# Performance work log

Measured on AMD Instinct MI355X. Metric: run time of the kernel, lower is better.

Reference implementation:

```python
import jax, jax.numpy as jnp
import numpy as np

N, E, F_IN, DIM, HEADS, L, G, NC = 10000, 160000, 512, 256, 4, 3, 16, 10
HID = HEADS * DIM  # 1024


def gat_layer(x, src, dst, W, a_src, a_dst, b):
    # x: [N, in], W: [in, H*D], a_src/a_dst: [H, D], b: [H*D]
    h = (x @ W).reshape(N, HEADS, DIM)                       # [N,H,D]
    e_src = jnp.einsum('nhd,hd->nh', h, a_src)               # [N,H]
    e_dst = jnp.einsum('nhd,hd->nh', h, a_dst)               # [N,H]
    e = jax.nn.leaky_relu(e_src[src] + e_dst[dst], 0.2)      # [E,H]
    # segment softmax over edges grouped by destination node
    emax = jax.ops.segment_max(e, dst, num_segments=N)       # [N,H]
    ee = jnp.exp(e - emax[dst])
    denom = jax.ops.segment_sum(ee, dst, num_segments=N)     # [N,H]
    alpha = ee / denom[dst]                                  # [E,H]
    msg = h[src] * alpha[:, :, None]                         # [E,H,D]
    out = jax.ops.segment_sum(msg, dst, num_segments=N)      # [N,H,D]
    return out.reshape(N, HID) + b


def setup_inputs() -> dict:
    key = jax.random.key(0)
    ks = jax.random.split(key, 12)
    x = jax.random.normal(ks[0], (N, F_IN), dtype=jnp.float32)
    edge_index = jax.random.randint(ks[1], (2, E), 0, N, dtype=jnp.int32)
    batch = jnp.sort(jax.random.randint(ks[2], (N,), 0, G, dtype=jnp.int32))
    s0 = 1.0 / np.sqrt(F_IN)
    s1 = 1.0 / np.sqrt(HID)
    sd = 1.0 / np.sqrt(DIM)
    W0 = jax.random.normal(ks[3], (F_IN, HID), dtype=jnp.float32) * s0
    W1 = jax.random.normal(ks[4], (HID, HID), dtype=jnp.float32) * s1
    W2 = jax.random.normal(ks[5], (HID, HID), dtype=jnp.float32) * s1
    a_src = jax.random.normal(ks[6], (L, HEADS, DIM), dtype=jnp.float32) * sd
    a_dst = jax.random.normal(ks[7], (L, HEADS, DIM), dtype=jnp.float32) * sd
    bias = jnp.zeros((L, HID), dtype=jnp.float32)
    fc_w = jax.random.normal(ks[8], (HID, NC), dtype=jnp.float32) * s1
    fc_b = jnp.zeros((NC,), dtype=jnp.float32)
    return {"x": x, "edge_index": edge_index, "batch": batch, "W0": W0,
            "W1": W1, "W2": W2, "a_src": a_src, "a_dst": a_dst,
            "bias": bias, "fc_w": fc_w, "fc_b": fc_b}


def reference(x, edge_index, batch, W0, W1, W2, a_src, a_dst, bias, fc_w, fc_b):
    # add self-loops (PyG GATConv default)
    loop = jnp.arange(N, dtype=edge_index.dtype)
    src = jnp.concatenate([edge_index[0], loop])
    dst = jnp.concatenate([edge_index[1], loop])
    Ws = [W0, W1, W2]
    h = x
    for l in range(L):
        h = gat_layer(h, src, dst, Ws[l], a_src[l], a_dst[l], bias[l])
        h = jax.nn.relu(h)  # Dropout(0.5) is identity in eval mode
    # global mean pool over graphs
    sums = jax.ops.segment_sum(h, batch, num_segments=G)            # [G,HID]
    cnts = jax.ops.segment_sum(jnp.ones((N,), h.dtype), batch, num_segments=G)
    pooled = sums / jnp.maximum(cnts, 1.0)[:, None]
    logits = pooled @ fc_w + fc_b
    return jax.nn.log_softmax(logits, axis=-1)
```

## Files before the change

### kernel.cpp

```cpp
#include <hip/hip_runtime.h>
#include <math.h>

#define NNODES 10000
#define HID    1024
#define NHEADS 4
#define NGRAPH 16
#define NCLS   10

typedef __attribute__((ext_vector_type(8))) short bf16x8;
typedef __attribute__((ext_vector_type(8))) ushort u16x8;
typedef __attribute__((ext_vector_type(4))) float f32x4;
typedef __attribute__((ext_vector_type(2))) float f32x2;

__device__ __forceinline__ ushort bf16r(float f) {
    union { float f; unsigned u; } x; x.f = f;
    unsigned r = x.u + 0x7FFFu + ((x.u >> 16) & 1u);
    return (ushort)(r >> 16);
}
__device__ __forceinline__ float bf16f(ushort u) {
    union { unsigned u; float f; } x; x.u = ((unsigned)u) << 16;
    return x.f;
}
__device__ __forceinline__ float leaky(float e) { return e > 0.f ? e : 0.2f * e; }


__global__ void k_hist_conv(const int* __restrict__ dstArr, int* __restrict__ counts,
                            const int* __restrict__ batch, int* __restrict__ gstart,
                            int* __restrict__ gend, int E, int N,
                            const float* __restrict__ x, ushort* __restrict__ xb16, int n4) {
    int e = blockIdx.x * 256 + threadIdx.x;
    int total = E + N;
    if (e < total) {
        int d = (e < E) ? dstArr[e] : (e - E);
        atomicAdd(&counts[d], 1);
    }
    if (e < N) {
        int g = batch[e];
        if (e == 0 || batch[e - 1] != g) gstart[g] = e;
        if (e == N - 1 || batch[e + 1] != g) gend[g] = e + 1;
    }
    if (e < n4) {
        float4 v = ((const float4*)x)[e];
        ushort4 o;
        o.x = bf16r(v.x); o.y = bf16r(v.y); o.z = bf16r(v.z); o.w = bf16r(v.w);
        ((ushort4*)xb16)[e] = o;
    }
}

__global__ __launch_bounds__(1024) void k_scan(const int* __restrict__ counts,
                                               int* __restrict__ row_ptr, int N) {
    __shared__ int lds[1024];
    int t = threadIdx.x;
    const int C = (N + 1023) / 1024;
    int base = t * C;
    int s = 0;
    for (int i = 0; i < C; ++i)
        if (base + i < N) s += counts[base + i];
    lds[t] = s;
    __syncthreads();
    for (int off = 1; off < 1024; off <<= 1) {
        int add = (t >= off) ? lds[t - off] : 0;
        __syncthreads();
        lds[t] += add;
        __syncthreads();
    }
    int run = lds[t] - s;
    for (int i = 0; i < C; ++i) {
        if (base + i < N) {
            row_ptr[base + i] = run;
            run += counts[base + i];
        }
    }
    if (t == 1023) row_ptr[N] = lds[1023];
}

__global__ void k_scatter(const int* __restrict__ srcArr, const int* __restrict__ dstArr,
                          const int* __restrict__ row_ptr, int* __restrict__ fill,
                          int* __restrict__ col, int E) {
    int e = blockIdx.x * 256 + threadIdx.x;
    int total = E + NNODES;
    if (e < total) {
        int s, d;
        if (e < E) { s = srcArr[e]; d = dstArr[e]; }
        else       { s = d = e - E; }
        int pos = row_ptr[d] + atomicAdd(&fill[d], 1);
        col[pos] = s;
    }
}

__global__ __launch_bounds__(256) void k_wT3(const float* __restrict__ W0,
                                             const float* __restrict__ W1,
                                             const float* __restrict__ W2,
                                             ushort* __restrict__ w0t,
                                             ushort* __restrict__ w1t,
                                             ushort* __restrict__ w2t) {
    __shared__ ushort tile[32][33];
    int z = blockIdx.z;
    const float* W = (z == 0) ? W0 : (z == 1) ? W1 : W2;
    ushort* Wt     = (z == 0) ? w0t : (z == 1) ? w1t : w2t;
    int K          = (z == 0) ? 512 : HID;
    int bx = blockIdx.x;
    int by = blockIdx.y;
    if (by * 32 >= K) return;
    int tx = threadIdx.x & 31, ty = threadIdx.x >> 5;
#pragma unroll
    for (int i = 0; i < 32; i += 8) {
        int k  = by * 32 + ty + i;
        int nn = bx * 32 + tx;
        tile[ty + i][tx] = bf16r(W[(size_t)k * HID + nn]);
    }
    __syncthreads();
#pragma unroll
    for (int i = 0; i < 32; i += 8) {
        int nn = bx * 32 + ty + i;
        int k  = by * 32 + tx;
        Wt[(size_t)nn * K + k] = tile[tx][ty + i];
    }
}


#define BM 128
#define BN 128
#define BK 64

__global__ __launch_bounds__(256) void k_gemm_bf16(const ushort* __restrict__ A,
                                                   const ushort* __restrict__ Bt,
                                                   unsigned char* __restrict__ proj8,
                                                   int M, int K,
                                                   const float* __restrict__ asrcL,
                                                   const float* __restrict__ adstL,
                                                   float* __restrict__ esrcP,
                                                   float* __restrict__ edstP) {
    __shared__ ushort As[BM * BK];
    __shared__ ushort Bs[BN * BK];
    const int t    = threadIdx.x;
    const int lane = t & 63;
    const int w    = t >> 6;
    const int wr   = w >> 1, wc = w & 1;
    const int bm   = blockIdx.y * BM;
    const int bn   = blockIdx.x * BN;

    f32x4 acc[4][4] = {};

    const int r_  = t >> 3;
    const int cp_ = t & 7;

    const ushort* aSrc[4];
    const ushort* bSrc[4];
#pragma unroll
    for (int i = 0; i < 4; ++i) {
        int r  = i * 32 + r_;
        int c  = cp_ ^ (r & 7);
        int ga = bm + r; if (ga >= M) ga = M - 1;
        aSrc[i] = &A[(size_t)ga * K + c * 8];
        bSrc[i] = &Bt[(size_t)(bn + r) * K + c * 8];
    }

    for (int k0 = 0; k0 < K; k0 += BK) {
        __syncthreads();
#pragma unroll
        for (int i = 0; i < 4; ++i) {
            int fc = i * 256 + t;
            __builtin_amdgcn_global_load_lds(
                (const __attribute__((address_space(1))) unsigned*)(aSrc[i] + k0),
                (__attribute__((address_space(3))) unsigned*)&As[fc * 8], 16, 0, 0);
            __builtin_amdgcn_global_load_lds(
                (const __attribute__((address_space(1))) unsigned*)(bSrc[i] + k0),
                (__attribute__((address_space(3))) unsigned*)&Bs[fc * 8], 16, 0, 0);
        }
        __syncthreads();

#pragma unroll
        for (int s = 0; s < 2; ++s) {
            const int kc = s * 4 + (lane >> 4);
            bf16x8 a[4], b[4];
#pragma unroll
            for (int m = 0; m < 4; ++m) {
                int row = wr * 64 + m * 16 + (lane & 15);
                int ch  = kc ^ (row & 7);
                a[m] = *(const bf16x8*)&As[row * BK + ch * 8];
            }
#pragma unroll
            for (int n = 0; n < 4; ++n) {
                int cl = wc * 64 + n * 16 + (lane & 15);
                int ch = kc ^ (cl & 7);
                b[n] = *(const bf16x8*)&Bs[cl * BK + ch * 8];
            }
#pragma unroll
            for (int m = 0; m < 4; ++m)
#pragma unroll
                for (int n = 0; n < 4; ++n)
                    acc[m][n] = __builtin_amdgcn_mfma_f32_16x16x32_bf16(a[m], b[n], acc[m][n], 0, 0, 0);
        }
    }

    const int hcol0 = bn + wc * 64;
    const int slot  = hcol0 >> 6;
    float as_[4], ad_[4];
#pragma unroll
    for (int n = 0; n < 4; ++n) {
        int coln = hcol0 + n * 16 + (lane & 15);
        as_[n] = asrcL[coln];
        ad_[n] = adstL[coln];
    }
#pragma unroll
    for (int m = 0; m < 4; ++m) {
        int row0 = bm + wr * 64 + m * 16 + (lane >> 4) * 4;
#pragma unroll
        for (int j = 0; j < 4; ++j) {
            int row = row0 + j;
            float ps = 0.f, pd = 0.f;
#pragma unroll
            for (int n = 0; n < 4; ++n) {
                float v = acc[m][n][j];
                ps += v * as_[n];
                pd += v * ad_[n];
                if (row < M) {
                    int r8 = __builtin_amdgcn_cvt_pk_fp8_f32(v, v, 0, false);
                    proj8[(size_t)row * HID + hcol0 + n * 16 + (lane & 15)] =
                        (unsigned char)(r8 & 0xFF);
                }
            }
#pragma unroll
            for (int off = 1; off < 16; off <<= 1) {
                ps += __shfl_xor(ps, off);
                pd += __shfl_xor(pd, off);
            }
            if ((lane & 15) == 0 && row < M) {
                esrcP[row * 16 + slot] = ps;
                edstP[row * 16 + slot] = pd;
            }
        }
    }
}


__global__ __launch_bounds__(256) void k_agg(const unsigned char* __restrict__ proj8,
                                             const float* __restrict__ esrcP,
                                             const float* __restrict__ edstP,
                                             const int* __restrict__ row_ptr,
                                             const int* __restrict__ col,
                                             const float* __restrict__ bias,
                                             ushort* __restrict__ hb16) {
    __shared__ float aLds[4][64][NHEADS];

    const int nb   = threadIdx.x >> 6;
    const int nid  = blockIdx.x * 4 + nb;
    const int lane = threadIdx.x & 63;
    const int h    = lane >> 4;
    const int beg  = row_ptr[nid], end = row_ptr[nid + 1];
    const int deg  = end - beg;
    const bool fast = (deg <= 64);

    const float4* edP = (const float4*)&edstP[(size_t)nid * 16];
    float4 eda = edP[0], edb = edP[1], edc = edP[2], edd = edP[3];
    const float ed0 = eda.x + eda.y + eda.z + eda.w;
    const float ed1 = edb.x + edb.y + edb.z + edb.w;
    const float ed2 = edc.x + edc.y + edc.z + edc.w;
    const float ed3 = edd.x + edd.y + edd.z + edd.w;
    float invh;

    if (fast) {
        float e0[4];
        const bool has = lane < deg;
        float d0 = 0.f, d1 = 0.f, d2 = 0.f, d3 = 0.f;
        if (has) {
            const float4* eP = (const float4*)&esrcP[(size_t)col[beg + lane] * 16];
            float4 sa = eP[0], sb = eP[1], sc = eP[2], sd = eP[3];
            e0[0] = __expf(leaky(sa.x + sa.y + sa.z + sa.w + ed0)); d0 = e0[0];
            e0[1] = __expf(leaky(sb.x + sb.y + sb.z + sb.w + ed1)); d1 = e0[1];
            e0[2] = __expf(leaky(sc.x + sc.y + sc.z + sc.w + ed2)); d2 = e0[2];
            e0[3] = __expf(leaky(sd.x + sd.y + sd.z + sd.w + ed3)); d3 = e0[3];
        }
#pragma unroll
        for (int off = 32; off > 0; off >>= 1) {
            d0 += __shfl_xor(d0, off); d1 += __shfl_xor(d1, off);
            d2 += __shfl_xor(d2, off); d3 += __shfl_xor(d3, off);
        }
        if (has) {
            float4 a4 = make_float4(e0[0] / d0, e0[1] / d1, e0[2] / d2, e0[3] / d3);
            *(float4*)&aLds[nb][lane][0] = a4;
        }
    } else {
        float d0 = 0.f, d1 = 0.f, d2 = 0.f, d3 = 0.f;
        for (int j = beg + lane; j < end; j += 64) {
            const float4* eP = (const float4*)&esrcP[(size_t)col[j] * 16];
            float4 sa = eP[0], sb = eP[1], sc = eP[2], sd = eP[3];
            d0 += __expf(leaky(sa.x + sa.y + sa.z + sa.w + ed0));
            d1 += __expf(leaky(sb.x + sb.y + sb.z + sb.w + ed1));
            d2 += __expf(leaky(sc.x + sc.y + sc.z + sc.w + ed2));
            d3 += __expf(leaky(sd.x + sd.y + sd.z + sd.w + ed3));
        }
#pragma unroll
        for (int off = 32; off > 0; off >>= 1) {
            d0 += __shfl_xor(d0, off); d1 += __shfl_xor(d1, off);
            d2 += __shfl_xor(d2, off); d3 += __shfl_xor(d3, off);
        }
        invh = 1.f / ((h == 0) ? d0 : (h == 1) ? d1 : (h == 2) ? d2 : d3);
    }

    const unsigned char* pbase = proj8 + lane * 16;
    float acc[16] = {};

#define FMA1(A, V)                                                           \
    {                                                                        \
        f32x2 q01_ = __builtin_amdgcn_cvt_pk_f32_fp8(V.x, false);            \
        f32x2 q23_ = __builtin_amdgcn_cvt_pk_f32_fp8(V.x, true);             \
        f32x2 q45_ = __builtin_amdgcn_cvt_pk_f32_fp8(V.y, false);            \
        f32x2 q67_ = __builtin_amdgcn_cvt_pk_f32_fp8(V.y, true);             \
        f32x2 q89_ = __builtin_amdgcn_cvt_pk_f32_fp8(V.z, false);            \
        f32x2 qAB_ = __builtin_amdgcn_cvt_pk_f32_fp8(V.z, true);             \
        f32x2 qCD_ = __builtin_amdgcn_cvt_pk_f32_fp8(V.w, false);            \
        f32x2 qEF_ = __builtin_amdgcn_cvt_pk_f32_fp8(V.w, true);             \
        acc[0]  += A * q01_[0]; acc[1]  += A * q01_[1];                      \
        acc[2]  += A * q23_[0]; acc[3]  += A * q23_[1];                      \
        acc[4]  += A * q45_[0]; acc[5]  += A * q45_[1];                      \
        acc[6]  += A * q67_[0]; acc[7]  += A * q67_[1];                      \
        acc[8]  += A * q89_[0]; acc[9]  += A * q89_[1];                      \
        acc[10] += A * qAB_[0]; acc[11] += A * qAB_[1];                      \
        acc[12] += A * qCD_[0]; acc[13] += A * qCD_[1];                      \
        acc[14] += A * qEF_[0]; acc[15] += A * qEF_[1];                      \
    }

    if (fast) {
#define LOADCHUNK(cb, A0, A1, A2, A3, V0, V1, V2, V3)                        \
    {                                                                        \
        int4 cc_ = *(const int4*)&col[cb];                                   \
        bool m0_ = ((cb) + 0 >= beg) & ((cb) + 0 < end);                     \
        bool m1_ = ((cb) + 1 >= beg) & ((cb) + 1 < end);                     \
        bool m2_ = ((cb) + 2 >= beg) & ((cb) + 2 < end);                     \
        bool m3_ = ((cb) + 3 >= beg) & ((cb) + 3 < end);                     \
        int s0_ = m0_ ? cc_.x : 0; int s1_ = m1_ ? cc_.y : 0;                \
        int s2_ = m2_ ? cc_.z : 0; int s3_ = m3_ ? cc_.w : 0;                \
        int l0_ = m0_ ? (cb) + 0 - beg : 0; int l1_ = m1_ ? (cb) + 1 - beg : 0; \
        int l2_ = m2_ ? (cb) + 2 - beg : 0; int l3_ = m3_ ? (cb) + 3 - beg : 0; \
        A0 = m0_ ? aLds[nb][l0_][h] : 0.f;                                   \
        A1 = m1_ ? aLds[nb][l1_][h] : 0.f;                                   \
        A2 = m2_ ? aLds[nb][l2_][h] : 0.f;                                   \
        A3 = m3_ ? aLds[nb][l3_][h] : 0.f;                                   \
        V0 = *(const uint4*)(pbase + (size_t)s0_ * HID);                     \
        V1 = *(const uint4*)(pbase + (size_t)s1_ * HID);                     \
        V2 = *(const uint4*)(pbase + (size_t)s2_ * HID);                     \
        V3 = *(const uint4*)(pbase + (size_t)s3_ * HID);                     \
    }
#define FMACHUNK(A0, A1, A2, A3, V0, V1, V2, V3)                             \
    { FMA1(A0, V0) FMA1(A1, V1) FMA1(A2, V2) FMA1(A3, V3) }

        int c = beg & ~3;
        float a0, a1, a2, a3;
        uint4 v0, v1, v2, v3;
        LOADCHUNK(c, a0, a1, a2, a3, v0, v1, v2, v3);
        for (c += 4; c < end; c += 4) {
            float na0, na1, na2, na3;
            uint4 nv0, nv1, nv2, nv3;
            LOADCHUNK(c, na0, na1, na2, na3, nv0, nv1, nv2, nv3);
            FMACHUNK(a0, a1, a2, a3, v0, v1, v2, v3);
            a0 = na0; a1 = na1; a2 = na2; a3 = na3;
            v0 = nv0; v1 = nv1; v2 = nv2; v3 = nv3;
        }
        FMACHUNK(a0, a1, a2, a3, v0, v1, v2, v3);
#undef LOADCHUNK
#undef FMACHUNK
    } else {
        const float edn = (h == 0) ? ed0 : (h == 1) ? ed1 : (h == 2) ? ed2 : ed3;
        for (int j = beg; j < end; ++j) {
            int s = col[j];
            float es = esrcP[(size_t)s * 16 + 4 * h]     + esrcP[(size_t)s * 16 + 4 * h + 1]
                     + esrcP[(size_t)s * 16 + 4 * h + 2] + esrcP[(size_t)s * 16 + 4 * h + 3];
            float a = __expf(leaky(es + edn)) * invh;
            uint4 v = *(const uint4*)(pbase + (size_t)s * HID);
            FMA1(a, v);
        }
    }
#undef FMA1

    u16x8 o0, o1;
#pragma unroll
    for (int i = 0; i < 8; ++i) {
        o0[i] = bf16r(fmaxf(acc[i]     + bias[lane * 16 + i],     0.f));
        o1[i] = bf16r(fmaxf(acc[8 + i] + bias[lane * 16 + 8 + i], 0.f));
    }
    *(u16x8*)&hb16[(size_t)nid * HID + lane * 16]     = o0;
    *(u16x8*)&hb16[(size_t)nid * HID + lane * 16 + 8] = o1;
}


#define PCHUNK 32
__global__ __launch_bounds__(256) void k_pool(const ushort* __restrict__ h,
                                              const int* __restrict__ batch,
                                              float* __restrict__ pooled, int N) {
    int c  = blockIdx.y * 256 + threadIdx.x;
    int n0 = blockIdx.x * PCHUNK;
    int n1 = n0 + PCHUNK; if (n1 > N) n1 = N;
    int g = batch[n0];
    float acc = 0.f;
    for (int n = n0; n < n1; ++n) {
        int gn = batch[n];
        if (gn != g) {
            atomicAdd(&pooled[g * HID + c], acc);
            acc = 0.f; g = gn;
        }
        acc += bf16f(h[(size_t)n * HID + c]);
    }
    atomicAdd(&pooled[g * HID + c], acc);
}

__global__ __launch_bounds__(256) void k_fc(const float* __restrict__ pooled,
                                            const int* __restrict__ gstart,
                                            const int* __restrict__ gend,
                                            const float* __restrict__ fcw,
                                            const float* __restrict__ fcb,
                                            float* __restrict__ out) {
    int g = blockIdx.x;
    int t = threadIdx.x;
    float invc = 1.f / fmaxf((float)(gend[g] - gstart[g]), 1.f);
    __shared__ float red[NCLS][256];
    float part[NCLS];
#pragma unroll
    for (int c = 0; c < NCLS; ++c) part[c] = 0.f;
    for (int k = t; k < HID; k += 256) {
        float v = pooled[g * HID + k] * invc;
#pragma unroll
        for (int c = 0; c < NCLS; ++c) part[c] += v * fcw[k * NCLS + c];
    }
#pragma unroll
    for (int c = 0; c < NCLS; ++c) red[c][t] = part[c];
    __syncthreads();
    for (int off = 128; off > 0; off >>= 1) {
        if (t < off) {
#pragma unroll
            for (int c = 0; c < NCLS; ++c) red[c][t] += red[c][t + off];
        }
        __syncthreads();
    }
    if (t == 0) {
        float logits[NCLS];
        float mx = -1e30f;
#pragma unroll
        for (int c = 0; c < NCLS; ++c) {
            logits[c] = red[c][0] + fcb[c];
            mx = fmaxf(mx, logits[c]);
        }
        float se = 0.f;
#pragma unroll
        for (int c = 0; c < NCLS; ++c) se += expf(logits[c] - mx);
        float lse = mx + logf(se);
#pragma unroll
        for (int c = 0; c < NCLS; ++c) out[g * NCLS + c] = logits[c] - lse;
    }
}


extern "C" void kernel_launch(void* const* d_in, const int* in_sizes, int n_in,
                              void* d_out, int out_size, void* d_ws, size_t ws_size,
                              hipStream_t stream) {
    const float* x    = (const float*)d_in[0];
    const int*   ei   = (const int*)d_in[1];
    const int*   batch= (const int*)d_in[2];
    const float* W0   = (const float*)d_in[3];
    const float* W1   = (const float*)d_in[4];
    const float* W2   = (const float*)d_in[5];
    const float* asrc = (const float*)d_in[6];
    const float* adst = (const float*)d_in[7];
    const float* bias = (const float*)d_in[8];
    const float* fcw  = (const float*)d_in[9];
    const float* fcb  = (const float*)d_in[10];
    float* out = (float*)d_out;

    const int E = in_sizes[1] / 2;
    const int N = NNODES;
    const int NE = E + N;
    const int N4 = N * 512 / 4;

    char* ws = (char*)d_ws;
    size_t off = 0;
    auto alloc = [&](size_t bytes) { void* p = ws + off; off += (bytes + 255) & ~(size_t)255; return p; };
    unsigned char* proj8 = (unsigned char*)alloc((size_t)N * HID);
    ushort* hb16   = (ushort*)alloc((size_t)N * HID * 2);
    ushort* xb16   = (ushort*)alloc((size_t)N * 512 * 2);
    ushort* w0t    = (ushort*)alloc((size_t)HID * 512 * 2);
    ushort* w1t    = (ushort*)alloc((size_t)HID * HID * 2);
    ushort* w2t    = (ushort*)alloc((size_t)HID * HID * 2);
    float*  esrcP  = (float*)alloc((size_t)N * 16 * 4);
    float*  edstP  = (float*)alloc((size_t)N * 16 * 4);
    int*    row_ptr= (int*)alloc((size_t)(N + 1) * 4);
    int*    col    = (int*)alloc((size_t)(NE + 16) * 4);
    size_t zstart = off;
    int*    counts  = (int*)alloc((size_t)N * 4);
    int*    fill    = (int*)alloc((size_t)N * 4);
    int*    gstart  = (int*)alloc(NGRAPH * 4);
    int*    gend    = (int*)alloc(NGRAPH * 4);
    float*  pooled  = (float*)alloc(NGRAPH * HID * 4);
    size_t zbytes = off - zstart;
    (void)ws_size;

    const int* srcArr = ei;
    const int* dstArr = ei + E;

    hipMemsetAsync(ws + zstart, 0, zbytes, stream);
    hipMemsetAsync(col + NE, 0, 16 * 4, stream);

    int nbHC = max((NE + 255) / 256, (N4 + 255) / 256);
    k_hist_conv<<<nbHC, 256, 0, stream>>>(dstArr, counts, batch, gstart, gend, E, N,
                                          x, xb16, N4);
    k_scan<<<1, 1024, 0, stream>>>(counts, row_ptr, N);
    int nbE = (NE + 255) / 256;
    k_scatter<<<nbE, 256, 0, stream>>>(srcArr, dstArr, row_ptr, fill, col, E);

    k_wT3<<<dim3(32, HID / 32, 3), 256, 0, stream>>>(W0, W1, W2, w0t, w1t, w2t);

    dim3 gemmGrid(HID / BN, (N + BM - 1) / BM);

    k_gemm_bf16<<<gemmGrid, 256, 0, stream>>>(xb16, w0t, proj8, N, 512,
                                              asrc + 0 * HID, adst + 0 * HID, esrcP, edstP);
    k_agg<<<N / 4, 256, 0, stream>>>(proj8, esrcP, edstP, row_ptr, col, bias + 0 * HID, hb16);

    k_gemm_bf16<<<gemmGrid, 256, 0, stream>>>(hb16, w1t, proj8, N, HID,
                                              asrc + 1 * HID, adst + 1 * HID, esrcP, edstP);
    k_agg<<<N / 4, 256, 0, stream>>>(proj8, esrcP, edstP, row_ptr, col, bias + 1 * HID, hb16);

    k_gemm_bf16<<<gemmGrid, 256, 0, stream>>>(hb16, w2t, proj8, N, HID,
                                              asrc + 2 * HID, adst + 2 * HID, esrcP, edstP);
    k_agg<<<N / 4, 256, 0, stream>>>(proj8, esrcP, edstP, row_ptr, col, bias + 2 * HID, hb16);

    dim3 poolGrid((N + PCHUNK - 1) / PCHUNK, HID / 256);
    k_pool<<<poolGrid, 256, 0, stream>>>(hb16, batch, pooled, N);
    k_fc<<<NGRAPH, 256, 0, stream>>>(pooled, gstart, gend, fcw, fcb, out);
}
```

Measured before the change: 247.7 us.

## Fuse weight transpose into preprocessing and mean-pool into last aggregation

Merges the weight transpose/bf16 conversion into the preprocessing kernel as extra blocks, removing one launch. Fuses global mean pooling into the final aggregation kernel: each block stages its four node outputs in shared memory and atomically adds them to the pooled sums, skipping the final hidden-state write and the separate pool kernel. This trades memory traffic for many more global float atomics and extra shared memory in every aggregation launch.

```diff
diff --git a/kernel.cpp b/kernel.cpp
--- a/kernel.cpp
+++ b/kernel.cpp
@@ -24,26 +24,58 @@
 __device__ __forceinline__ float leaky(float e) { return e > 0.f ? e : 0.2f * e; }
 
 
-__global__ void k_hist_conv(const int* __restrict__ dstArr, int* __restrict__ counts,
-                            const int* __restrict__ batch, int* __restrict__ gstart,
-                            int* __restrict__ gend, int E, int N,
-                            const float* __restrict__ x, ushort* __restrict__ xb16, int n4) {
-    int e = blockIdx.x * 256 + threadIdx.x;
-    int total = E + N;
-    if (e < total) {
-        int d = (e < E) ? dstArr[e] : (e - E);
-        atomicAdd(&counts[d], 1);
-    }
-    if (e < N) {
-        int g = batch[e];
-        if (e == 0 || batch[e - 1] != g) gstart[g] = e;
-        if (e == N - 1 || batch[e + 1] != g) gend[g] = e + 1;
-    }
-    if (e < n4) {
-        float4 v = ((const float4*)x)[e];
-        ushort4 o;
-        o.x = bf16r(v.x); o.y = bf16r(v.y); o.z = bf16r(v.z); o.w = bf16r(v.w);
-        ((ushort4*)xb16)[e] = o;
+__global__ __launch_bounds__(256) void k_pre(const int* __restrict__ dstArr, int* __restrict__ counts,
+                                             const int* __restrict__ batch, int* __restrict__ gstart,
+                                             int* __restrict__ gend, int E, int N,
+                                             const float* __restrict__ x, ushort* __restrict__ xb16, int n4,
+                                             const float* __restrict__ W0, const float* __restrict__ W1,
+                                             const float* __restrict__ W2,
+                                             ushort* __restrict__ w0t, ushort* __restrict__ w1t,
+                                             ushort* __restrict__ w2t, int nbConv) {
+    __shared__ ushort tile[32][33];
+    int b = blockIdx.x;
+    if (b < nbConv) {
+        int e = b * 256 + threadIdx.x;
+        int total = E + N;
+        if (e < total) {
+            int d = (e < E) ? dstArr[e] : (e - E);
+            atomicAdd(&counts[d], 1);
+        }
+        if (e < N) {
+            int g = batch[e];
+            if (e == 0 || batch[e - 1] != g) gstart[g] = e;
+            if (e == N - 1 || batch[e + 1] != g) gend[g] = e + 1;
+        }
+        if (e < n4) {
+            float4 v = ((const float4*)x)[e];
+            ushort4 o;
+            o.x = bf16r(v.x); o.y = bf16r(v.y); o.z = bf16r(v.z); o.w = bf16r(v.w);
+            ((ushort4*)xb16)[e] = o;
+        }
+    } else {
+        int bb = b - nbConv;
+        int z  = bb >> 10;
+        int rem = bb & 1023;
+        int bx = rem & 31, by = rem >> 5;
+        const float* W = (z == 0) ? W0 : (z == 1) ? W1 : W2;
+        ushort* Wt     = (z == 0) ? w0t : (z == 1) ? w1t : w2t;
+        int K          = (z == 0) ? 512 : HID;
+        if (by * 32 < K) {
+            int tx = threadIdx.x & 31, ty = threadIdx.x >> 5;
+#pragma unroll
+            for (int i = 0; i < 32; i += 8) {
+                int k  = by * 32 + ty + i;
+                int nn = bx * 32 + tx;
+                tile[ty + i][tx] = bf16r(W[(size_t)k * HID + nn]);
+            }
+            __syncthreads();
+#pragma unroll
+            for (int i = 0; i < 32; i += 8) {
+                int nn = bx * 32 + ty + i;
+                int k  = by * 32 + tx;
+                Wt[(size_t)nn * K + k] = tile[tx][ty + i];
+            }
+        }
     }
 }
 
@@ -88,36 +120,6 @@
     }
 }
 
-__global__ __launch_bounds__(256) void k_wT3(const float* __restrict__ W0,
-                                             const float* __restrict__ W1,
-                                             const float* __restrict__ W2,
-                                             ushort* __restrict__ w0t,
-                                             ushort* __restrict__ w1t,
-                                             ushort* __restrict__ w2t) {
-    __shared__ ushort tile[32][33];
-    int z = blockIdx.z;
-    const float* W = (z == 0) ? W0 : (z == 1) ? W1 : W2;
-    ushort* Wt     = (z == 0) ? w0t : (z == 1) ? w1t : w2t;
-    int K          = (z == 0) ? 512 : HID;
-    int bx = blockIdx.x;
-    int by = blockIdx.y;
-    if (by * 32 >= K) return;
-    int tx = threadIdx.x & 31, ty = threadIdx.x >> 5;
-#pragma unroll
-    for (int i = 0; i < 32; i += 8) {
-        int k  = by * 32 + ty + i;
-        int nn = bx * 32 + tx;
-        tile[ty + i][tx] = bf16r(W[(size_t)k * HID + nn]);
-    }
-    __syncthreads();
-#pragma unroll
-    for (int i = 0; i < 32; i += 8) {
-        int nn = bx * 32 + ty + i;
-        int k  = by * 32 + tx;
-        Wt[(size_t)nn * K + k] = tile[tx][ty + i];
-    }
-}
-
 
 #define BM 128
 #define BN 128
@@ -241,8 +243,12 @@
                                              const int* __restrict__ row_ptr,
                                              const int* __restrict__ col,
                                              const float* __restrict__ bias,
-                                             ushort* __restrict__ hb16) {
+                                             ushort* __restrict__ hb16,
+                                             const int* __restrict__ batch,
+                                             float* __restrict__ pooled, int doPool) {
     __shared__ float aLds[4][64][NHEADS];
+    __shared__ float sbuf[4][HID];
+    __shared__ int   gsh[4];
 
     const int nb   = threadIdx.x >> 6;
     const int nid  = blockIdx.x * 4 + nb;
@@ -380,30 +386,33 @@
         o0[i] = bf16r(fmaxf(acc[i]     + bias[lane * 16 + i],     0.f));
         o1[i] = bf16r(fmaxf(acc[8 + i] + bias[lane * 16 + 8 + i], 0.f));
     }
-    *(u16x8*)&hb16[(size_t)nid * HID + lane * 16]     = o0;
-    *(u16x8*)&hb16[(size_t)nid * HID + lane * 16 + 8] = o1;
-}
-
-
-#define PCHUNK 32
-__global__ __launch_bounds__(256) void k_pool(const ushort* __restrict__ h,
-                                              const int* __restrict__ batch,
-                                              float* __restrict__ pooled, int N) {
-    int c  = blockIdx.y * 256 + threadIdx.x;
-    int n0 = blockIdx.x * PCHUNK;
-    int n1 = n0 + PCHUNK; if (n1 > N) n1 = N;
-    int g = batch[n0];
-    float acc = 0.f;
-    for (int n = n0; n < n1; ++n) {
-        int gn = batch[n];
-        if (gn != g) {
-            atomicAdd(&pooled[g * HID + c], acc);
-            acc = 0.f; g = gn;
-        }
-        acc += bf16f(h[(size_t)n * HID + c]);
-    }
-    atomicAdd(&pooled[g * HID + c], acc);
-}
+    if (!doPool) {
+        *(u16x8*)&hb16[(size_t)nid * HID + lane * 16]     = o0;
+        *(u16x8*)&hb16[(size_t)nid * HID + lane * 16 + 8] = o1;
+    } else {
+#pragma unroll
+        for (int i = 0; i < 8; ++i) {
+            sbuf[nb][lane * 16 + i]     = bf16f((ushort)o0[i]);
+            sbuf[nb][lane * 16 + 8 + i] = bf16f((ushort)o1[i]);
+        }
+        if (lane == 0) gsh[nb] = batch[nid];
+        __syncthreads();
+        int g0 = gsh[0], g1 = gsh[1], g2 = gsh[2], g3 = gsh[3];
+        bool same = (g0 == g1) & (g1 == g2) & (g2 == g3);
+        for (int c = threadIdx.x; c < HID; c += 256) {
+            if (same) {
+                atomicAdd(&pooled[g0 * HID + c],
+                          sbuf[0][c] + sbuf[1][c] + sbuf[2][c] + sbuf[3][c]);
+            } else {
+                atomicAdd(&pooled[g0 * HID + c], sbuf[0][c]);
+                atomicAdd(&pooled[g1 * HID + c], sbuf[1][c]);
+                atomicAdd(&pooled[g2 * HID + c], sbuf[2][c]);
+                atomicAdd(&pooled[g3 * HID + c], sbuf[3][c]);
+            }
+        }
+    }
+}
+
 
 __global__ __launch_bounds__(256) void k_fc(const float* __restrict__ pooled,
                                             const int* __restrict__ gstart,
@@ -500,30 +509,29 @@
     hipMemsetAsync(ws + zstart, 0, zbytes, stream);
     hipMemsetAsync(col + NE, 0, 16 * 4, stream);
 
-    int nbHC = max((NE + 255) / 256, (N4 + 255) / 256);
-    k_hist_conv<<<nbHC, 256, 0, stream>>>(dstArr, counts, batch, gstart, gend, E, N,
-                                          x, xb16, N4);
+    int nbConv = max((NE + 255) / 256, (N4 + 255) / 256);
+    k_pre<<<nbConv + 3072, 256, 0, stream>>>(dstArr, counts, batch, gstart, gend, E, N,
+                                             x, xb16, N4, W0, W1, W2, w0t, w1t, w2t, nbConv);
     k_scan<<<1, 1024, 0, stream>>>(counts, row_ptr, N);
     int nbE = (NE + 255) / 256;
     k_scatter<<<nbE, 256, 0, stream>>>(srcArr, dstArr, row_ptr, fill, col, E);
 
-    k_wT3<<<dim3(32, HID / 32, 3), 256, 0, stream>>>(W0, W1, W2, w0t, w1t, w2t);
-
     dim3 gemmGrid(HID / BN, (N + BM - 1) / BM);
 
     k_gemm_bf16<<<gemmGrid, 256, 0, stream>>>(xb16, w0t, proj8, N, 512,
                                               asrc + 0 * HID, adst + 0 * HID, esrcP, edstP);
-    k_agg<<<N / 4, 256, 0, stream>>>(proj8, esrcP, edstP, row_ptr, col, bias + 0 * HID, hb16);
+    k_agg<<<N / 4, 256, 0, stream>>>(proj8, esrcP, edstP, row_ptr, col, bias + 0 * HID,
+                                     hb16, batch, pooled, 0);
 
     k_gemm_bf16<<<gemmGrid, 256, 0, stream>>>(hb16, w1t, proj8, N, HID,
                                               asrc + 1 * HID, adst + 1 * HID, esrcP, edstP);
-    k_agg<<<N / 4, 256, 0, stream>>>(proj8, esrcP, edstP, row_ptr, col, bias + 1 * HID, hb16);
+    k_agg<<<N / 4, 256, 0, stream>>>(proj8, esrcP, edstP, row_ptr, col, bias + 1 * HID,
+                                     hb16, batch, pooled, 0);
 
     k_gemm_bf16<<<gemmGrid, 256, 0, stream>>>(hb16, w2t, proj8, N, HID,
                                               asrc + 2 * HID, adst + 2 * HID, esrcP, edstP);
-    k_agg<<<N / 4, 256, 0, stream>>>(proj8, esrcP, edstP, row_ptr, col, bias + 2 * HID, hb16);
-
-    dim3 poolGrid((N + PCHUNK - 1) / PCHUNK, HID / 256);
-    k_pool<<<poolGrid, 256, 0, stream>>>(hb16, batch, pooled, N);
+    k_agg<<<N / 4, 256, 0, stream>>>(proj8, esrcP, edstP, row_ptr, col, bias + 2 * HID,
+                                     hb16, batch, pooled, 1);
+
     k_fc<<<NGRAPH, 256, 0, stream>>>(pooled, gstart, gend, fcw, fcb, out);
 }
```

Result: faster. 239.7 us (-3.3%).
